# Kernel optimization log

Hardware: AMD Instinct MI355X
Metric: run time of the kernel (lower is better)

Reference implementation:

```python
import jax, jax.numpy as jnp
import numpy as np

N_NODES = 100000
N_EDGES = 1600000
IN_DIM, HID_DIM, OUT_DIM = 128, 64, 40


def setup_inputs() -> dict:
    key = jax.random.key(0)
    k = jax.random.split(key, 6)
    feats = jax.random.normal(k[0], (N_NODES, IN_DIM), dtype=jnp.float32)
    src = jax.random.randint(k[1], (N_EDGES,), 0, N_NODES)
    dst = jax.random.randint(k[2], (N_EDGES,), 0, N_NODES)
    # Glorot-ish init for the two GraphConv weights
    W1 = jax.random.normal(k[3], (IN_DIM, HID_DIM), dtype=jnp.float32) * (2.0 / (IN_DIM + HID_DIM)) ** 0.5
    b1 = jnp.zeros((HID_DIM,), dtype=jnp.float32)
    W2 = jax.random.normal(k[4], (HID_DIM, OUT_DIM), dtype=jnp.float32) * (2.0 / (HID_DIM + OUT_DIM)) ** 0.5
    b2 = jnp.zeros((OUT_DIM,), dtype=jnp.float32)
    return {"feats": feats, "W1": W1, "b1": b1, "W2": W2, "b2": b2, "src": src, "dst": dst}


def _graph_conv(h, W, b, src, dst, n):
    # DGL GraphConv, norm='both': out = D_dst^{-1/2} * A^T * (D_src^{-1/2} * h) W + b
    # (weight applied before aggregation since in_feats > out_feats for both layers)
    ones_e = jnp.ones(src.shape, dtype=h.dtype)
    deg_out = jax.ops.segment_sum(ones_e, src, num_segments=n)
    deg_in = jax.ops.segment_sum(ones_e, dst, num_segments=n)
    norm_src = jnp.clip(deg_out, 1.0) ** -0.5  # [N]
    norm_dst = jnp.clip(deg_in, 1.0) ** -0.5   # [N]
    h = h * norm_src[:, None]
    h = h @ W                                   # [N, out]
    m = jax.ops.segment_sum(h[src], dst, num_segments=n)  # gather-scatter over edges
    return m * norm_dst[:, None] + b


def reference(feats, W1, b1, W2, b2, src, dst):
    n = feats.shape[0]
    # layer 0: GraphConv with relu activation (dropout is identity in eval)
    h1 = jax.nn.relu(_graph_conv(feats, W1, b1, src, dst, n))
    # layer 1: GraphConv, no activation
    h2 = _graph_conv(h1, W2, b2, src, dst, n)
    # GCN.forward returns (h_list, h); h_list holds the hidden layer output
    return (h1, h2)
```

## Files before the change

### kernel.cpp

```cpp
#include <hip/hip_runtime.h>
#include <hip/hip_bf16.h>

constexpr int N_NODES = 100000;
constexpr int N_EDGES = 1600000;
constexpr int IN_DIM  = 128;
constexpr int HID_DIM = 64;
constexpr int OUT_DIM = 40;

constexpr int BK_SHIFT = 9;
constexpr int NBKT = (N_NODES + 511) >> 9;
constexpr int ECAP = 9216;
constexpr int TILE = 2048;
constexpr int NTILES = (N_EDGES + TILE - 1) / TILE;
constexpr int GEMM_BLK = (N_NODES + 63) / 64;

typedef __attribute__((ext_vector_type(8))) short short8;
typedef __attribute__((ext_vector_type(4))) float f32x4;

__device__ inline float bf2f(unsigned int u16) {
  union { float f; unsigned int i; } c;
  c.i = u16 << 16;
  return c.f;
}

__device__ inline unsigned short f2bf(float f) {
  union { float f; unsigned int u; } c; c.f = f;
  unsigned int u = c.u + 0x7fffu + ((c.u >> 16) & 1u);
  return (unsigned short)(u >> 16);
}

__global__ void k_init(const float* __restrict__ W1, const float* __restrict__ W2,
                       unsigned short* __restrict__ Bfrag1, unsigned short* __restrict__ Bfrag2,
                       int* __restrict__ gcur) {
  int tid = threadIdx.x;
  for (int i = tid; i < 2 * NBKT; i += 256) gcur[i] = 0;
  for (int idx = tid; idx < 4 * 4 * 64 * 8; idx += 256) {
    int j = idx & 7;
    int lane = (idx >> 3) & 63;
    int nt = (idx >> 9) & 3;
    int ks = idx >> 11;
    int k = ks * 32 + 8 * (lane >> 4) + j;
    int col = nt * 16 + (lane & 15);
    Bfrag1[idx] = f2bf(W1[k * HID_DIM + col]);
  }
  for (int idx = tid; idx < 2 * 3 * 64 * 8; idx += 256) {
    int j = idx & 7;
    int lane = (idx >> 3) & 63;
    int nt = (idx >> 9) % 3;
    int ks = idx / (3 * 512);
    int k = ks * 32 + 8 * (lane >> 4) + j;
    int col = nt * 16 + (lane & 15);
    Bfrag2[idx] = (col < OUT_DIM) ? f2bf(W2[k * OUT_DIM + col]) : (unsigned short)0;
  }
}

__global__ __launch_bounds__(256) void k_part(const int* __restrict__ src,
                                              const int* __restrict__ dst,
                                              int* __restrict__ gcur,
                                              int* __restrict__ gcur2,
                                              unsigned int* __restrict__ pairs,
                                              unsigned short* __restrict__ spart) {
  __shared__ int scnt[NBKT], soff[NBKT], gbase[NBKT];
  __shared__ int scnt2[NBKT], soff2[NBKT], gbase2[NBKT];
  __shared__ unsigned int sord[TILE];
  __shared__ unsigned char sordB[TILE];
  __shared__ unsigned short sordS[TILE];
  __shared__ unsigned char sordSB[TILE];
  int tid = threadIdx.x;
  int tileBase = blockIdx.x * TILE;
  int tcnt = N_EDGES - tileBase; if (tcnt > TILE) tcnt = TILE;
  if (tid < NBKT) { scnt[tid] = 0; scnt2[tid] = 0; }
  __syncthreads();
  int s_[8], d_[8], pos_[8], pos2_[8];
#pragma unroll
  for (int t = 0; t < 8; ++t) {
    int idx = tileBase + t * 256 + tid;
    if (idx < N_EDGES) {
      s_[t] = src[idx];
      d_[t] = dst[idx];
      pos_[t]  = atomicAdd(&scnt[d_[t] >> BK_SHIFT], 1);
      pos2_[t] = atomicAdd(&scnt2[s_[t] >> BK_SHIFT], 1);
    }
  }
  __syncthreads();
  if (tid == 0) {
    int acc = 0, acc2 = 0;
    for (int i = 0; i < NBKT; ++i) {
      soff[i] = acc;   acc  += scnt[i];
      soff2[i] = acc2; acc2 += scnt2[i];
    }
  }
  __syncthreads();
  if (tid < NBKT) {
    int c = scnt[tid];  gbase[tid]  = c ? atomicAdd(&gcur[tid], c)  : 0;
    int c2 = scnt2[tid]; gbase2[tid] = c2 ? atomicAdd(&gcur2[tid], c2) : 0;
  }
#pragma unroll
  for (int t = 0; t < 8; ++t) {
    int idx = tileBase + t * 256 + tid;
    if (idx < N_EDGES) {
      int b  = d_[t] >> BK_SHIFT;
      int b2 = s_[t] >> BK_SHIFT;
      int p  = soff[b] + pos_[t];
      int p2 = soff2[b2] + pos2_[t];
      sord[p]  = (unsigned)s_[t] | ((unsigned)(d_[t] & 511) << 17);
      sordB[p] = (unsigned char)b;
      sordS[p2]  = (unsigned short)(s_[t] & 511);
      sordSB[p2] = (unsigned char)b2;
    }
  }
  __syncthreads();
  for (int i = tid; i < tcnt; i += 256) {
    int b = sordB[i];
    int g = gbase[b] + (i - soff[b]);
    if (g < ECAP) pairs[(size_t)b * ECAP + g] = sord[i];
  }
  for (int i = tid; i < tcnt; i += 256) {
    int b = sordSB[i];
    int g = gbase2[b] + (i - soff2[b]);
    if (g < ECAP) spart[(size_t)b * ECAP + g] = sordS[i];
  }
}

__global__ __launch_bounds__(256) void k_csrdeg(const unsigned int* __restrict__ pairs,
                                                const unsigned short* __restrict__ spart,
                                                const int* __restrict__ gcur,
                                                const int* __restrict__ gcur2,
                                                int* __restrict__ startg,
                                                int* __restrict__ cntg,
                                                float* __restrict__ norm_dst,
                                                float* __restrict__ norm_src,
                                                int* __restrict__ esrc) {
  __shared__ int cnt[512];
  __shared__ int off[512];
  __shared__ int cur[512];
  __shared__ int wsum[256];
  __shared__ int esrcL[ECAP];
  int tid = threadIdx.x;
  if (blockIdx.x >= NBKT) {
    int b = blockIdx.x - NBKT;
    int node0 = b << BK_SHIFT;
    int nNodes = N_NODES - node0; if (nNodes > 512) nNodes = 512;
    int E = gcur2[b]; if (E > ECAP) E = ECAP;
    cnt[tid] = 0; cnt[tid + 256] = 0;
    __syncthreads();
    const unsigned short* sp = spart + (size_t)b * ECAP;
    for (int i = tid; i < E; i += 256) atomicAdd(&cnt[sp[i]], 1);
    __syncthreads();
    for (int j = tid; j < nNodes; j += 256) {
      int c = cnt[j];
      norm_src[node0 + j] = rsqrtf((float)(c < 1 ? 1 : c));
    }
    return;
  }
  int b = blockIdx.x;
  int node0 = b << BK_SHIFT;
  int nNodes = N_NODES - node0; if (nNodes > 512) nNodes = 512;
  int E = gcur[b]; if (E > ECAP) E = ECAP;
  cnt[tid] = 0; cnt[tid + 256] = 0;
  __syncthreads();
  const unsigned int* pp = pairs + (size_t)b * ECAP;
  for (int i = tid; i < E; i += 256) atomicAdd(&cnt[pp[i] >> 17], 1);
  __syncthreads();
  int v0 = cnt[tid * 2], v1 = cnt[tid * 2 + 1];
  int s = v0 + v1;
  wsum[tid] = s; __syncthreads();
  for (int o = 1; o < 256; o <<= 1) {
    int x = (tid >= o) ? wsum[tid - o] : 0;
    __syncthreads();
    wsum[tid] += x;
    __syncthreads();
  }
  int excl = wsum[tid] - s;
  off[tid * 2] = excl;     cur[tid * 2] = excl;
  off[tid * 2 + 1] = excl + v0; cur[tid * 2 + 1] = excl + v0;
  __syncthreads();
  for (int i = tid; i < E; i += 256) {
    unsigned p = pp[i];
    int pos = atomicAdd(&cur[p >> 17], 1);
    esrcL[pos] = (int)(p & 0x1FFFFu);
  }
  __syncthreads();
  int base = b * ECAP;
  for (int i = tid; i < E; i += 256) esrc[base + i] = esrcL[i];
  for (int j = tid; j < nNodes; j += 256) {
    int c = cnt[j];
    startg[node0 + j] = base + off[j];
    cntg[node0 + j] = c;
    norm_dst[node0 + j] = rsqrtf((float)(c < 1 ? 1 : c));
  }
}

__global__ __launch_bounds__(256) void k_gemm1_mfma(
    const float* __restrict__ feats, const uint4* __restrict__ Bfrag1,
    const float* __restrict__ norm_src, __hip_bfloat16* __restrict__ t1) {
  int tid = threadIdx.x;
  int w = tid >> 6, lane = tid & 63;
  int row0 = blockIdx.x * 64 + w * 16;
  int arow = row0 + (lane & 15);
  int arowc = arow < N_NODES ? arow : N_NODES - 1;
  int half = lane >> 4;

  const float4* fr = (const float4*)(feats + (size_t)arowc * IN_DIM);
  f32x4 acc[4] = {{0.f,0.f,0.f,0.f},{0.f,0.f,0.f,0.f},{0.f,0.f,0.f,0.f},{0.f,0.f,0.f,0.f}};
#pragma unroll
  for (int ks = 0; ks < 4; ++ks) {
    float4 p0 = fr[ks * 8 + 2 * half];
    float4 p1 = fr[ks * 8 + 2 * half + 1];
    short8 a;
    a[0] = (short)f2bf(p0.x); a[1] = (short)f2bf(p0.y);
    a[2] = (short)f2bf(p0.z); a[3] = (short)f2bf(p0.w);
    a[4] = (short)f2bf(p1.x); a[5] = (short)f2bf(p1.y);
    a[6] = (short)f2bf(p1.z); a[7] = (short)f2bf(p1.w);
#pragma unroll
    for (int nt = 0; nt < 4; ++nt) {
      uint4 bu = Bfrag1[(ks * 4 + nt) * 64 + lane];
      short8 b = *(const short8*)&bu;
      acc[nt] = __builtin_amdgcn_mfma_f32_16x16x32_bf16(a, b, acc[nt], 0, 0, 0);
    }
  }
  int col = lane & 15;
  int rbase = row0 + half * 4;
#pragma unroll
  for (int r = 0; r < 4; ++r) {
    int grow = rbase + r;
    if (grow < N_NODES) {
      float ns = norm_src[grow];
#pragma unroll
      for (int nt = 0; nt < 4; ++nt) {
        unsigned short h = f2bf(acc[nt][r] * ns);
        *((unsigned short*)t1 + (size_t)grow * HID_DIM + nt * 16 + col) = h;
      }
    }
  }
}

__global__ __launch_bounds__(256) void k_gemm2_mfma(
    const float* __restrict__ h1, const uint4* __restrict__ Bfrag2,
    const float* __restrict__ norm_src, __hip_bfloat16* __restrict__ t2) {
  int tid = threadIdx.x;
  int w = tid >> 6, lane = tid & 63;
  int row0 = blockIdx.x * 64 + w * 16;
  int arow = row0 + (lane & 15);
  int arowc = arow < N_NODES ? arow : N_NODES - 1;
  int half = lane >> 4;

  const float4* hr = (const float4*)(h1 + (size_t)arowc * HID_DIM);
  float ns = norm_src[arowc];
  f32x4 acc[3] = {{0.f,0.f,0.f,0.f},{0.f,0.f,0.f,0.f},{0.f,0.f,0.f,0.f}};
#pragma unroll
  for (int ks = 0; ks < 2; ++ks) {
    float4 p0 = hr[ks * 8 + 2 * half];
    float4 p1 = hr[ks * 8 + 2 * half + 1];
    short8 a;
    a[0] = (short)f2bf(p0.x * ns); a[1] = (short)f2bf(p0.y * ns);
    a[2] = (short)f2bf(p0.z * ns); a[3] = (short)f2bf(p0.w * ns);
    a[4] = (short)f2bf(p1.x * ns); a[5] = (short)f2bf(p1.y * ns);
    a[6] = (short)f2bf(p1.z * ns); a[7] = (short)f2bf(p1.w * ns);
#pragma unroll
    for (int nt = 0; nt < 3; ++nt) {
      uint4 bu = Bfrag2[(ks * 3 + nt) * 64 + lane];
      short8 b = *(const short8*)&bu;
      acc[nt] = __builtin_amdgcn_mfma_f32_16x16x32_bf16(a, b, acc[nt], 0, 0, 0);
    }
  }
  int col = lane & 15;
  int rbase = row0 + half * 4;
#pragma unroll
  for (int r = 0; r < 4; ++r) {
    int grow = rbase + r;
    if (grow < N_NODES) {
#pragma unroll
      for (int nt = 0; nt < 3; ++nt) {
        int gcol = nt * 16 + col;
        if (gcol < OUT_DIM)
          *((unsigned short*)t2 + (size_t)grow * OUT_DIM + gcol) = f2bf(acc[nt][r]);
      }
    }
  }
}

__global__ __launch_bounds__(256) void k_agg1(
    const uint2* __restrict__ t1, const int* __restrict__ startg,
    const int* __restrict__ cntg, const int* __restrict__ esrc,
    const float* __restrict__ norm_dst, const float4* __restrict__ b1,
    float4* __restrict__ out1) {
  int tid = threadIdx.x;
  int g = tid >> 4, q = tid & 15;
  int n = blockIdx.x * 16 + g;
  int s0 = startg[n];
  int c  = cntg[n];
  const int* bk = esrc + s0;
  float a0 = 0.f, a1 = 0.f, a2 = 0.f, a3 = 0.f;
  for (int i = 0; i < c; i += 8) {
#pragma unroll
    for (int t = 0; t < 8; ++t) {
      int ii = i + t;
      bool ok = ii < c;
      int s = bk[ok ? ii : 0];
      uint2 v = t1[(size_t)s * 16 + q];
      unsigned vx = ok ? v.x : 0u;
      unsigned vy = ok ? v.y : 0u;
      a0 += bf2f(vx & 0xffffu);
      a1 += bf2f(vx >> 16);
      a2 += bf2f(vy & 0xffffu);
      a3 += bf2f(vy >> 16);
    }
  }
  float nd = norm_dst[n];
  float4 bb = b1[q];
  float4 r;
  r.x = fmaxf(a0 * nd + bb.x, 0.f);
  r.y = fmaxf(a1 * nd + bb.y, 0.f);
  r.z = fmaxf(a2 * nd + bb.z, 0.f);
  r.w = fmaxf(a3 * nd + bb.w, 0.f);
  out1[(size_t)n * 16 + q] = r;
}

__global__ __launch_bounds__(256) void k_agg2(
    const uint2* __restrict__ t2, const int* __restrict__ startg,
    const int* __restrict__ cntg, const int* __restrict__ esrc,
    const float* __restrict__ norm_dst, const float4* __restrict__ b2,
    float4* __restrict__ out2) {
  int idx = blockIdx.x * blockDim.x + threadIdx.x;
  int n = idx / 10;
  int q = idx - n * 10;
  if (n >= N_NODES) return;
  int s0 = startg[n];
  int c  = cntg[n];
  const int* bk = esrc + s0;
  float a0 = 0.f, a1 = 0.f, a2 = 0.f, a3 = 0.f;
  for (int i = 0; i < c; i += 8) {
#pragma unroll
    for (int t = 0; t < 8; ++t) {
      int ii = i + t;
      bool ok = ii < c;
      int s = bk[ok ? ii : 0];
      uint2 v = t2[(size_t)s * 10 + q];
      unsigned vx = ok ? v.x : 0u;
      unsigned vy = ok ? v.y : 0u;
      a0 += bf2f(vx & 0xffffu);
      a1 += bf2f(vx >> 16);
      a2 += bf2f(vy & 0xffffu);
      a3 += bf2f(vy >> 16);
    }
  }
  float nd = norm_dst[n];
  float4 bb = b2[q];
  float4 r;
  r.x = a0 * nd + bb.x;
  r.y = a1 * nd + bb.y;
  r.z = a2 * nd + bb.z;
  r.w = a3 * nd + bb.w;
  out2[(size_t)n * 10 + q] = r;
}

extern "C" void kernel_launch(void* const* d_in, const int* in_sizes, int n_in,
                              void* d_out, int out_size, void* d_ws, size_t ws_size,
                              hipStream_t stream) {
  const float* feats = (const float*)d_in[0];
  const float* W1    = (const float*)d_in[1];
  const float* b1    = (const float*)d_in[2];
  const float* W2    = (const float*)d_in[3];
  const float* b2    = (const float*)d_in[4];
  const int*   src   = (const int*)d_in[5];
  const int*   dst   = (const int*)d_in[6];

  float* out  = (float*)d_out;
  float* out1 = out;
  float* out2 = out + (size_t)N_NODES * HID_DIM;

  __hip_bfloat16* t1 = (__hip_bfloat16*)d_ws;
  __hip_bfloat16* t2 = t1 + (size_t)N_NODES * HID_DIM;
  unsigned int* pairs = (unsigned int*)(t2 + (size_t)N_NODES * OUT_DIM);
  unsigned short* spart = (unsigned short*)(pairs + (size_t)NBKT * ECAP);
  int* esrc   = (int*)(spart + (size_t)NBKT * ECAP);
  unsigned short* Bfrag1 = (unsigned short*)(esrc + (size_t)NBKT * ECAP);
  unsigned short* Bfrag2 = Bfrag1 + 4 * 4 * 64 * 8;
  int* startg = (int*)(Bfrag2 + 2 * 3 * 64 * 8);
  int* cntg   = startg + N_NODES;
  float* norm_src = (float*)(cntg + N_NODES);
  float* norm_dst = norm_src + N_NODES;
  int* gcur  = (int*)(norm_dst + N_NODES);
  int* gcur2 = gcur + NBKT;

  k_init<<<1, 256, 0, stream>>>(W1, W2, Bfrag1, Bfrag2, gcur);
  k_part<<<NTILES, 256, 0, stream>>>(src, dst, gcur, gcur2, pairs, spart);
  k_csrdeg<<<2 * NBKT, 256, 0, stream>>>(pairs, spart, gcur, gcur2,
                                         startg, cntg, norm_dst, norm_src, esrc);

  k_gemm1_mfma<<<GEMM_BLK, 256, 0, stream>>>(feats, (const uint4*)Bfrag1, norm_src, t1);
  k_agg1<<<N_NODES / 16, 256, 0, stream>>>((const uint2*)t1, startg, cntg, esrc,
                                           norm_dst, (const float4*)b1, (float4*)out1);
  k_gemm2_mfma<<<GEMM_BLK, 256, 0, stream>>>(out1, (const uint4*)Bfrag2, norm_src, t2);
  k_agg2<<<(N_NODES * 10 + 255) / 256, 256, 0, stream>>>((const uint2*)t2, startg, cntg, esrc,
                                                         norm_dst, (const float4*)b2, (float4*)out2);
}
```

Before: 155.3 us.

## Fuse layer-2 GEMM into layer-1 aggregation and parallelize bucket prefix scan

```diff
diff --git a/kernel.cpp b/kernel.cpp
--- a/kernel.cpp
+++ b/kernel.cpp
@@ -62,6 +62,7 @@
                                               unsigned short* __restrict__ spart) {
   __shared__ int scnt[NBKT], soff[NBKT], gbase[NBKT];
   __shared__ int scnt2[NBKT], soff2[NBKT], gbase2[NBKT];
+  __shared__ int sc1[256], sc2[256];
   __shared__ unsigned int sord[TILE];
   __shared__ unsigned char sordB[TILE];
   __shared__ unsigned short sordS[TILE];
@@ -83,18 +84,24 @@
     }
   }
   __syncthreads();
-  if (tid == 0) {
-    int acc = 0, acc2 = 0;
-    for (int i = 0; i < NBKT; ++i) {
-      soff[i] = acc;   acc  += scnt[i];
-      soff2[i] = acc2; acc2 += scnt2[i];
-    }
-  }
-  __syncthreads();
+  int v1 = (tid < NBKT) ? scnt[tid] : 0;
+  int v2 = (tid < NBKT) ? scnt2[tid] : 0;
+  sc1[tid] = v1; sc2[tid] = v2;
+  __syncthreads();
+  for (int o = 1; o < 256; o <<= 1) {
+    int x1 = (tid >= o) ? sc1[tid - o] : 0;
+    int x2 = (tid >= o) ? sc2[tid - o] : 0;
+    __syncthreads();
+    sc1[tid] += x1; sc2[tid] += x2;
+    __syncthreads();
+  }
   if (tid < NBKT) {
-    int c = scnt[tid];  gbase[tid]  = c ? atomicAdd(&gcur[tid], c)  : 0;
-    int c2 = scnt2[tid]; gbase2[tid] = c2 ? atomicAdd(&gcur2[tid], c2) : 0;
-  }
+    soff[tid]  = sc1[tid] - v1;
+    soff2[tid] = sc2[tid] - v2;
+    gbase[tid]  = v1 ? atomicAdd(&gcur[tid],  v1) : 0;
+    gbase2[tid] = v2 ? atomicAdd(&gcur2[tid], v2) : 0;
+  }
+  __syncthreads();
 #pragma unroll
   for (int t = 0; t < 8; ++t) {
     int idx = tileBase + t * 256 + tid;
@@ -235,56 +242,13 @@
   }
 }
 
-__global__ __launch_bounds__(256) void k_gemm2_mfma(
-    const float* __restrict__ h1, const uint4* __restrict__ Bfrag2,
-    const float* __restrict__ norm_src, __hip_bfloat16* __restrict__ t2) {
-  int tid = threadIdx.x;
-  int w = tid >> 6, lane = tid & 63;
-  int row0 = blockIdx.x * 64 + w * 16;
-  int arow = row0 + (lane & 15);
-  int arowc = arow < N_NODES ? arow : N_NODES - 1;
-  int half = lane >> 4;
-
-  const float4* hr = (const float4*)(h1 + (size_t)arowc * HID_DIM);
-  float ns = norm_src[arowc];
-  f32x4 acc[3] = {{0.f,0.f,0.f,0.f},{0.f,0.f,0.f,0.f},{0.f,0.f,0.f,0.f}};
-#pragma unroll
-  for (int ks = 0; ks < 2; ++ks) {
-    float4 p0 = hr[ks * 8 + 2 * half];
-    float4 p1 = hr[ks * 8 + 2 * half + 1];
-    short8 a;
-    a[0] = (short)f2bf(p0.x * ns); a[1] = (short)f2bf(p0.y * ns);
-    a[2] = (short)f2bf(p0.z * ns); a[3] = (short)f2bf(p0.w * ns);
-    a[4] = (short)f2bf(p1.x * ns); a[5] = (short)f2bf(p1.y * ns);
-    a[6] = (short)f2bf(p1.z * ns); a[7] = (short)f2bf(p1.w * ns);
-#pragma unroll
-    for (int nt = 0; nt < 3; ++nt) {
-      uint4 bu = Bfrag2[(ks * 3 + nt) * 64 + lane];
-      short8 b = *(const short8*)&bu;
-      acc[nt] = __builtin_amdgcn_mfma_f32_16x16x32_bf16(a, b, acc[nt], 0, 0, 0);
-    }
-  }
-  int col = lane & 15;
-  int rbase = row0 + half * 4;
-#pragma unroll
-  for (int r = 0; r < 4; ++r) {
-    int grow = rbase + r;
-    if (grow < N_NODES) {
-#pragma unroll
-      for (int nt = 0; nt < 3; ++nt) {
-        int gcol = nt * 16 + col;
-        if (gcol < OUT_DIM)
-          *((unsigned short*)t2 + (size_t)grow * OUT_DIM + gcol) = f2bf(acc[nt][r]);
-      }
-    }
-  }
-}
-
-__global__ __launch_bounds__(256) void k_agg1(
+__global__ __launch_bounds__(256) void k_agg1g2(
     const uint2* __restrict__ t1, const int* __restrict__ startg,
     const int* __restrict__ cntg, const int* __restrict__ esrc,
-    const float* __restrict__ norm_dst, const float4* __restrict__ b1,
-    float4* __restrict__ out1) {
+    const float* __restrict__ norm_dst, const float* __restrict__ norm_src,
+    const float4* __restrict__ b1, const uint4* __restrict__ Bfrag2,
+    float4* __restrict__ out1, __hip_bfloat16* __restrict__ t2) {
+  __shared__ unsigned short h1s[16][64];
   int tid = threadIdx.x;
   int g = tid >> 4, q = tid & 15;
   int n = blockIdx.x * 16 + g;
@@ -309,12 +273,42 @@
   }
   float nd = norm_dst[n];
   float4 bb = b1[q];
-  float4 r;
-  r.x = fmaxf(a0 * nd + bb.x, 0.f);
-  r.y = fmaxf(a1 * nd + bb.y, 0.f);
-  r.z = fmaxf(a2 * nd + bb.z, 0.f);
-  r.w = fmaxf(a3 * nd + bb.w, 0.f);
-  out1[(size_t)n * 16 + q] = r;
+  float h0 = fmaxf(a0 * nd + bb.x, 0.f);
+  float h1 = fmaxf(a1 * nd + bb.y, 0.f);
+  float h2 = fmaxf(a2 * nd + bb.z, 0.f);
+  float h3 = fmaxf(a3 * nd + bb.w, 0.f);
+  out1[(size_t)n * 16 + q] = make_float4(h0, h1, h2, h3);
+  float ns = norm_src[n];
+  unsigned lo = (unsigned)f2bf(h0 * ns) | ((unsigned)f2bf(h1 * ns) << 16);
+  unsigned hi = (unsigned)f2bf(h2 * ns) | ((unsigned)f2bf(h3 * ns) << 16);
+  *(uint2*)&h1s[g][q * 4] = make_uint2(lo, hi);
+  __syncthreads();
+  if (tid < 64) {
+    int lane = tid;
+    int r = lane & 15, half = lane >> 4;
+    f32x4 acc[3] = {{0.f,0.f,0.f,0.f},{0.f,0.f,0.f,0.f},{0.f,0.f,0.f,0.f}};
+#pragma unroll
+    for (int ks = 0; ks < 2; ++ks) {
+      short8 a = *(const short8*)&h1s[r][ks * 32 + 8 * half];
+#pragma unroll
+      for (int nt = 0; nt < 3; ++nt) {
+        uint4 bu = Bfrag2[(ks * 3 + nt) * 64 + lane];
+        short8 b = *(const short8*)&bu;
+        acc[nt] = __builtin_amdgcn_mfma_f32_16x16x32_bf16(a, b, acc[nt], 0, 0, 0);
+      }
+    }
+    int col = lane & 15;
+#pragma unroll
+    for (int r2 = 0; r2 < 4; ++r2) {
+      int node = blockIdx.x * 16 + half * 4 + r2;
+#pragma unroll
+      for (int nt = 0; nt < 3; ++nt) {
+        int j = nt * 16 + col;
+        if (j < OUT_DIM)
+          *((unsigned short*)t2 + (size_t)node * OUT_DIM + j) = f2bf(acc[nt][r2]);
+      }
+    }
+  }
 }
 
 __global__ __launch_bounds__(256) void k_agg2(
@@ -390,9 +384,9 @@
                                          startg, cntg, norm_dst, norm_src, esrc);
 
   k_gemm1_mfma<<<GEMM_BLK, 256, 0, stream>>>(feats, (const uint4*)Bfrag1, norm_src, t1);
-  k_agg1<<<N_NODES / 16, 256, 0, stream>>>((const uint2*)t1, startg, cntg, esrc,
-                                           norm_dst, (const float4*)b1, (float4*)out1);
-  k_gemm2_mfma<<<GEMM_BLK, 256, 0, stream>>>(out1, (const uint4*)Bfrag2, norm_src, t2);
+  k_agg1g2<<<N_NODES / 16, 256, 0, stream>>>((const uint2*)t1, startg, cntg, esrc,
+                                             norm_dst, norm_src, (const float4*)b1,
+                                             (const uint4*)Bfrag2, (float4*)out1, t2);
   k_agg2<<<(N_NODES * 10 + 255) / 256, 256, 0, stream>>>((const uint2*)t2, startg, cntg, esrc,
                                                          norm_dst, (const float4*)b2, (float4*)out2);
 }
```

Measured after the change: 147.8 us. -4.8%, faster.
